# Optimization experiments

Hardware: AMD Instinct MI355X
Metric: run time of the kernel (lower is better)

## Reference

```python
import math
import jax, jax.numpy as jnp
import numpy as np

B, C_IN, H, W = 32, 96, 64, 64
OUT = 128
EXC = int(OUT * 0.8)   # 102 excitatory channels
INH = OUT - EXC        # 26 inhibitory channels
K = 5
PAD = 2                # kernel//2 so all stages keep spatial size


def _sm_kernel(kernel_size=5, sigma_e=1.2, sigma_i=1.4):
    c = kernel_size // 2
    xx, yy = np.meshgrid(np.arange(kernel_size), np.arange(kernel_size), indexing='ij')
    xx = xx.astype(np.float32) - c
    yy = yy.astype(np.float32) - c
    ge = np.exp(-(xx ** 2 + yy ** 2) / (2 * sigma_e ** 2))
    gi = np.exp(-(xx ** 2 + yy ** 2) / (2 * sigma_i ** 2))
    dog = ge / (2 * math.pi * sigma_e ** 2) - gi / (2 * math.pi * sigma_i ** 2)
    dog = dog / dog[c, c]
    return jnp.asarray(dog[None, None], dtype=jnp.float32)  # [1,1,K,K]


def setup_inputs() -> dict:
    key = jax.random.key(0)
    k1, k2, k3, k4 = jax.random.split(key, 4)
    wr = 25.0 / math.sqrt(C_IN * K * K)
    x = jax.random.normal(k1, (B, C_IN, H, W), jnp.float32)
    w_ee = wr * jnp.abs(jax.random.normal(k2, (EXC, C_IN, K, K), jnp.float32))
    w_ei = wr * jnp.abs(jax.random.normal(k3, (INH, EXC, K, K), jnp.float32))
    w_ie = -wr * jnp.abs(jax.random.normal(k4, (EXC, INH, K, K), jnp.float32))
    return {"x": x, "w_ee": w_ee, "w_ei": w_ei, "w_ie": w_ie, "sm_kernel": _sm_kernel()}


def _reflect_pad(x, p):
    if p == 0:
        return x
    return jnp.pad(x, ((0, 0), (0, 0), (p, p), (p, p)), mode='reflect')


def _conv(x, w, pad=0, groups=1):
    return jax.lax.conv_general_dilated(
        x, w, window_strides=(1, 1), padding=[(pad, pad), (pad, pad)],
        dimension_numbers=('NCHW', 'OIHW', 'NCHW'), feature_group_count=groups)


def _forward(x, w_ee, w_ei, w_ie, sm_kernel):
    y_e = _conv(_reflect_pad(x, PAD), w_ee)                 # [B,EXC,H,W], act=Identity
    y_i = jax.nn.relu(_conv(_reflect_pad(y_e, PAD), w_ei))  # [B,INH,H,W]
    y_ie = _conv(_reflect_pad(y_i, PAD), w_ie)              # [B,EXC,H,W]
    y = y_e + y_ie
    # depthwise surround-modulation conv (zero padding, as in F.conv2d)
    w_sm = jnp.tile(sm_kernel, (EXC, 1, 1, 1))              # [EXC,1,K,K]
    y = _conv(y, w_sm, pad=K // 2, groups=EXC)
    return y, y_e, y_i


def reference(x, w_ee, w_ei, w_ie, sm_kernel):
    y, y_e, y_i = _forward(x, w_ee, w_ei, w_ie, sm_kernel)

    # --- hard WTA masks (winner channel per (b,h,w) position) ---
    win_e = jnp.argmax(y_e, axis=1)                                        # [B,H,W]
    mask_e = (jnp.arange(EXC)[None, :, None, None] == win_e[:, None]).astype(y_e.dtype)
    y_wta_e = y_e * mask_e
    win_i = jnp.argmax(jnp.abs(y_i), axis=1)
    mask_i = (jnp.arange(INH)[None, :, None, None] == win_i[:, None]).astype(y_i.dtype)
    y_wta_i = y_i * mask_i

    # --- transpose-conv outer-product trick; with same-size feature maps the
    # conv collapses to a 1x1 full correlation over (b,h,w) -> einsum ---
    yx_ee = jnp.einsum('bchw,behw->ec', x, y_wta_e)[:, :, None, None]      # [EXC,C_IN,1,1]
    yx_ei = jnp.einsum('behw,bihw->ie', y_wta_e, y_wta_i)[:, :, None, None]  # [INH,EXC,1,1]
    yx_ie = jnp.einsum('bihw,behw->ei', y_wta_i, y)[:, :, None, None]      # [EXC,INH,1,1]

    yu_e = jnp.sum(y_wta_e, axis=(0, 2, 3))[:, None, None, None]           # [EXC,1,1,1]
    yu_i = jnp.sum(jnp.abs(y_wta_i), axis=(0, 2, 3))[:, None, None, None]  # [INH,1,1,1]

    upd_ee = yx_ee - yu_e * w_ee   # broadcasts to [EXC,C_IN,K,K]
    upd_ei = yx_ei - yu_i * w_ei
    upd_ie = yx_ie - yu_e * w_ie
    upd_ee = upd_ee / (jnp.abs(upd_ee).max() + 1e-8)
    upd_ei = upd_ei / (jnp.abs(upd_ei).max() + 1e-8)
    upd_ie = upd_ie / (jnp.abs(upd_ie).max() + 1e-8)

    return (y, upd_ee, upd_ei, upd_ie)
```

## Files before the change

### kernel.cpp

```cpp
#include <hip/hip_runtime.h>

#define B_    32
#define CIN_  96
#define EXC_  102
#define INH_  26
#define HH    64
#define WW    64
#define HW_   4096
#define NPOS  (B_*HW_)

typedef short bf8 __attribute__((ext_vector_type(8)));
typedef float f32x4 __attribute__((ext_vector_type(4)));

__device__ __forceinline__ int refl(int i) {
    if (i < 0) i = -i;
    if (i > 63) i = 126 - i;
    return i;
}

__device__ __forceinline__ short f2bf(float f) {
    unsigned u = __float_as_uint(f);
    return (short)((u + 0x7fffu + ((u >> 16) & 1u)) >> 16);
}

template<int C, int CPAD>
__global__ __launch_bounds__(256) void pack_nhwc(
    const float* __restrict__ src, short* __restrict__ dst)
{
    const int b = blockIdx.z;
    const int pos = blockIdx.x*64 + (threadIdx.x & 63);
    const int cg0 = threadIdx.x >> 6;
    for (int cg = cg0; cg < CPAD/8; cg += 4) {
        bf8 v;
#pragma unroll
        for (int j = 0; j < 8; ++j) {
            int c = cg*8 + j;
            float f = (c < C) ? src[((size_t)b*C + c)*HW_ + pos] : 0.f;
            v[j] = f2bf(f);
        }
        *(bf8*)(&dst[((size_t)b*HW_ + pos)*CPAD + cg*8]) = v;
    }
}

template<int N, int C, int NPAD, int CPAD>
__global__ void pack_w(const float* __restrict__ src, short* __restrict__ dst)
{
    int idx = blockIdx.x*256 + threadIdx.x;
    if (idx >= 25*NPAD*CPAD) return;
    int tap = idx / (NPAD*CPAD);
    int rem = idx - tap*NPAD*CPAD;
    int n = rem / CPAD, c = rem - n*CPAD;
    float f = (n < N && c < C) ? src[((size_t)n*C + c)*25 + tap] : 0.f;
    dst[idx] = f2bf(f);
}

template<int CPAD, int NPAD, int NT, int COUT, int NCHUNK, bool RELU, bool ADDIN>
__global__ __launch_bounds__(256, 2) void conv_mfma(
    const short* __restrict__ src, const short* __restrict__ wgt,
    const float* __restrict__ addin, float* __restrict__ out)
{
    __shared__ __align__(16) short sA[400*40];
    const int t  = threadIdx.x;
    const int bx = blockIdx.x;
    const int b  = blockIdx.z;
    const int h0 = (bx >> 2) * 16;
    const int w0 = (bx &  3) * 16;
    const int lane = t & 63;
    const int wv = t >> 6;
    const int nh = lane & 15;
    const int q  = lane >> 4;

    int goff[7], loff[7];
#pragma unroll
    for (int s = 0; s < 7; ++s) {
        int i = t + 256*s;
        if (i < 1600) {
            int rec = i >> 2, seg = i & 3;
            int lh = rec / 20, lw = rec - lh*20;
            int gh = refl(h0 - 2 + lh), gw = refl(w0 - 2 + lw);
            goff[s] = (b*HW_ + gh*WW + gw) * CPAD + seg*8;
            loff[s] = rec*40 + seg*8;
        } else { goff[s] = 0; loff[s] = -1; }
    }

    f32x4 acc[4][NT];
#pragma unroll
    for (int mt = 0; mt < 4; ++mt)
#pragma unroll
        for (int nt = 0; nt < NT; ++nt) {
            f32x4 z = {0.f, 0.f, 0.f, 0.f};
            acc[mt][nt] = z;
        }

    int abase[4];
#pragma unroll
    for (int mt = 0; mt < 4; ++mt)
        abase[mt] = ((wv*4 + mt)*20 + nh)*40 + q*8;

    for (int ck = 0; ck < NCHUNK; ++ck) {
        const int c0 = ck*32;
        __syncthreads();
#pragma unroll
        for (int s = 0; s < 7; ++s)
            if (loff[s] >= 0)
                *(bf8*)(&sA[loff[s]]) = *(const bf8*)(&src[goff[s] + c0]);
        __syncthreads();
        const short* wch = wgt + c0 + nh*CPAD + q*8;
        for (int dh = 0; dh < 5; ++dh) {
#pragma unroll
            for (int dw = 0; dw < 5; ++dw) {
                const int tap = dh*5 + dw;
                bf8 bfr[NT];
#pragma unroll
                for (int nt = 0; nt < NT; ++nt)
                    bfr[nt] = *(const bf8*)(&wch[(size_t)(tap*NPAD + nt*16)*CPAD]);
                bf8 afr[4];
#pragma unroll
                for (int mt = 0; mt < 4; ++mt)
                    afr[mt] = *(const bf8*)(&sA[abase[mt] + (dh*20 + dw)*40]);
#pragma unroll
                for (int mt = 0; mt < 4; ++mt)
#pragma unroll
                    for (int nt = 0; nt < NT; ++nt)
                        acc[mt][nt] = __builtin_amdgcn_mfma_f32_16x16x32_bf16(
                            afr[mt], bfr[nt], acc[mt][nt], 0, 0, 0);
            }
        }
    }

#pragma unroll
    for (int mt = 0; mt < 4; ++mt) {
        const int rowi = h0 + wv*4 + mt;
#pragma unroll
        for (int nt = 0; nt < NT; ++nt) {
            const int chn = nt*16 + nh;
            if (chn < COUT) {
                size_t obase = ((size_t)(b*COUT + chn))*HW_ + rowi*WW + w0 + q*4;
#pragma unroll
                for (int r = 0; r < 4; ++r) {
                    float v = acc[mt][nt][r];
                    if (RELU) v = fmaxf(v, 0.f);
                    if (ADDIN) v += addin[obase + r];
                    out[obase + r] = v;
                }
            }
        }
    }
}

__global__ __launch_bounds__(256) void smconv_v2(
    const float* __restrict__ in, const float* __restrict__ sm,
    float* __restrict__ out)
{
    __shared__ __align__(16) float sx[36*36];
    const int tid = threadIdx.x;
    const int tile = blockIdx.x;
    const int e = blockIdx.y;
    const int b = blockIdx.z;
    const int h0 = (tile >> 1) * 32, w0 = (tile & 1) * 32;
    const int r  = tid >> 3;
    const int cg = (tid & 7) * 4;
    const float* inc = in + ((size_t)(b*EXC_ + e))*HW_;
#pragma unroll
    for (int it = 0; it < 6; ++it) {
        int i = tid + it*256;
        if (i < 1296) {
            int lh = i / 36, lw = i - lh*36;
            int gh = h0 - 2 + lh, gw = w0 - 2 + lw;
            float v = 0.f;
            if (gh >= 0 && gh < HH && gw >= 0 && gw < WW) v = inc[gh*WW + gw];
            sx[i] = v;
        }
    }
    __syncthreads();
    float a0 = 0.f, a1 = 0.f, a2 = 0.f, a3 = 0.f;
#pragma unroll
    for (int kh = 0; kh < 5; ++kh) {
        const float4* rowp = (const float4*)(sx + (r + kh)*36 + cg);
        float4 v0 = rowp[0], v1 = rowp[1];
        float xv[8] = {v0.x, v0.y, v0.z, v0.w, v1.x, v1.y, v1.z, v1.w};
#pragma unroll
        for (int kw = 0; kw < 5; ++kw) {
            float wv = sm[kh*5 + kw];
            a0 = fmaf(xv[kw+0], wv, a0);
            a1 = fmaf(xv[kw+1], wv, a1);
            a2 = fmaf(xv[kw+2], wv, a2);
            a3 = fmaf(xv[kw+3], wv, a3);
        }
    }
    size_t oidx = ((size_t)(b*EXC_ + e))*HW_ + (h0 + r)*WW + w0 + cg;
    *(float4*)(out + oidx) = make_float4(a0, a1, a2, a3);
}

__global__ void wta_kernel(const float* __restrict__ in, int* __restrict__ win,
                           float* __restrict__ val, int C, int use_abs)
{
    int p = blockIdx.x*256 + threadIdx.x;
    int b = p >> 12, hw = p & 4095;
    const float* base = in + ((size_t)b*C)*HW_ + hw;
    float bestv = base[0];
    float bestk = use_abs ? fabsf(bestv) : bestv;
    int besti = 0;
    for (int c = 1; c < C; ++c) {
        float v = base[(size_t)c*HW_];
        float key = use_abs ? fabsf(v) : v;
        if (key > bestk) { bestk = key; bestv = v; besti = c; }
    }
    win[p] = besti;
    val[p] = bestv;
}

__global__ __launch_bounds__(256) void scatter_ee_kernel(
    const float* __restrict__ x, const int* __restrict__ win_e,
    const float* __restrict__ val_e, float* __restrict__ yx_ee,
    float* __restrict__ yu_e)
{
    __shared__ float s_yx[EXC_*CIN_];
    __shared__ float s_yu[EXC_];
    for (int i = threadIdx.x; i < EXC_*CIN_; i += 256) s_yx[i] = 0.f;
    if (threadIdx.x < EXC_) s_yu[threadIdx.x] = 0.f;
    __syncthreads();
    int p0 = blockIdx.x * 512;
    for (int it = 0; it < 2; ++it) {
        int p = p0 + it*256 + threadIdx.x;
        int b = p >> 12, hw = p & 4095;
        int wi = win_e[p]; float v = val_e[p];
        atomicAdd(&s_yu[wi], v);
        const float* xb = x + ((size_t)b*CIN_)*HW_ + hw;
        float* row = s_yx + wi*CIN_;
        for (int c = 0; c < CIN_; ++c)
            atomicAdd(&row[c], v * xb[(size_t)c*HW_]);
    }
    __syncthreads();
    for (int i = threadIdx.x; i < EXC_*CIN_; i += 256) atomicAdd(&yx_ee[i], s_yx[i]);
    if (threadIdx.x < EXC_) atomicAdd(&yu_e[threadIdx.x], s_yu[threadIdx.x]);
}

__global__ __launch_bounds__(256) void scatter_ei_kernel(
    const int* __restrict__ win_e, const float* __restrict__ val_e,
    const int* __restrict__ win_i, const float* __restrict__ val_i,
    float* __restrict__ yx_ei, float* __restrict__ yu_i)
{
    __shared__ float s[INH_*EXC_ + INH_];
    for (int i = threadIdx.x; i < INH_*EXC_ + INH_; i += 256) s[i] = 0.f;
    __syncthreads();
    int p0 = blockIdx.x * 1024;
    for (int it = 0; it < 4; ++it) {
        int p = p0 + it*256 + threadIdx.x;
        int we = win_e[p]; float ve = val_e[p];
        int wi = win_i[p]; float vi = val_i[p];
        atomicAdd(&s[wi*EXC_ + we], ve*vi);
        atomicAdd(&s[INH_*EXC_ + wi], fabsf(vi));
    }
    __syncthreads();
    for (int i = threadIdx.x; i < INH_*EXC_ + INH_; i += 256) {
        float v = s[i];
        if (v != 0.f) {
            if (i < INH_*EXC_) atomicAdd(&yx_ei[i], v);
            else               atomicAdd(&yu_i[i - INH_*EXC_], v);
        }
    }
}

__global__ __launch_bounds__(256) void scatter_ie_kernel(
    const float* __restrict__ y, const int* __restrict__ win_i,
    const float* __restrict__ val_i, float* __restrict__ yx_ie)
{
    __shared__ float s[EXC_*INH_];
    for (int i = threadIdx.x; i < EXC_*INH_; i += 256) s[i] = 0.f;
    __syncthreads();
    int p0 = blockIdx.x * 512;
    for (int it = 0; it < 2; ++it) {
        int p = p0 + it*256 + threadIdx.x;
        int b = p >> 12, hw = p & 4095;
        int wi = win_i[p]; float v = val_i[p];
        if (v != 0.f) {
            const float* yb = y + ((size_t)b*EXC_)*HW_ + hw;
            for (int e = 0; e < EXC_; ++e)
                atomicAdd(&s[e*INH_ + wi], v * yb[(size_t)e*HW_]);
        }
    }
    __syncthreads();
    for (int i = threadIdx.x; i < EXC_*INH_; i += 256) atomicAdd(&yx_ie[i], s[i]);
}

__global__ void upd_absmax_kernel(const float* __restrict__ yx,
    const float* __restrict__ yu, const float* __restrict__ w,
    int E, int C, unsigned int* __restrict__ amax)
{
    __shared__ unsigned int sm_;
    if (threadIdx.x == 0) sm_ = 0u;
    __syncthreads();
    int n = E*C*25;
    float m = 0.f;
    for (int idx = blockIdx.x*256 + threadIdx.x; idx < n; idx += gridDim.x*256) {
        int ec = idx / 25;
        int e = ec / C;
        float v = yx[ec] - yu[e]*w[idx];
        m = fmaxf(m, fabsf(v));
    }
    atomicMax(&sm_, __float_as_uint(m));
    __syncthreads();
    if (threadIdx.x == 0) atomicMax(amax, sm_);
}

__global__ void upd_write_kernel(const float* __restrict__ yx,
    const float* __restrict__ yu, const float* __restrict__ w,
    int E, int C, const unsigned int* __restrict__ amax,
    float* __restrict__ out)
{
    int n = E*C*25;
    int idx = blockIdx.x*256 + threadIdx.x;
    if (idx >= n) return;
    int ec = idx / 25;
    int e = ec / C;
    float v = yx[ec] - yu[e]*w[idx];
    float mx = __uint_as_float(*amax);
    out[idx] = v / (mx + 1e-8f);
}

extern "C" void kernel_launch(void* const* d_in, const int* in_sizes, int n_in,
                              void* d_out, int out_size, void* d_ws, size_t ws_size,
                              hipStream_t stream)
{
    const float* x    = (const float*)d_in[0];
    const float* w_ee = (const float*)d_in[1];
    const float* w_ei = (const float*)d_in[2];
    const float* w_ie = (const float*)d_in[3];
    const float* smk  = (const float*)d_in[4];
    float* out = (float*)d_out;

    float* y_e = (float*)d_ws;
    float* y_i = y_e + (size_t)B_*EXC_*HW_;
    short* R   = (short*)(y_i + (size_t)B_*INH_*HW_);
    short* wee = R + (size_t)16777216;
    short* wei = wee + 268800;
    short* wie = wei + 102400;
    int*   win_e = (int*)(wie + 89600);
    float* val_e = (float*)(win_e + NPOS);
    int*   win_i = (int*)(val_e + NPOS);
    float* val_i = (float*)(win_i + NPOS);
    float* yx_ee = val_i + NPOS;
    float* yx_ei = yx_ee + EXC_*CIN_;
    float* yx_ie = yx_ei + INH_*EXC_;
    float* yu_e  = yx_ie + EXC_*INH_;
    float* yu_i  = yu_e + EXC_;
    unsigned int* amax = (unsigned int*)(yu_i + INH_);

    hipMemsetAsync(yx_ee, 0,
        (size_t)(EXC_*CIN_ + INH_*EXC_ + EXC_*INH_ + EXC_ + INH_ + 3)*sizeof(float),
        stream);

    pack_w<EXC_, CIN_, 112, 96><<<(25*112*96 + 255)/256, 256, 0, stream>>>(w_ee, wee);
    pack_w<INH_, EXC_, 32, 128><<<(25*32*128 + 255)/256, 256, 0, stream>>>(w_ei, wei);
    pack_w<EXC_, INH_, 112, 32><<<(25*112*32 + 255)/256, 256, 0, stream>>>(w_ie, wie);
    pack_nhwc<CIN_, 96><<<dim3(64, 1, B_), 256, 0, stream>>>(x, R);

    conv_mfma<96, 112, 7, EXC_, 3, false, false>
        <<<dim3(16, 1, B_), 256, 0, stream>>>(R, wee, nullptr, y_e);
    wta_kernel<<<NPOS/256, 256, 0, stream>>>(y_e, win_e, val_e, EXC_, 0);

    pack_nhwc<EXC_, 128><<<dim3(64, 1, B_), 256, 0, stream>>>(y_e, R);
    conv_mfma<128, 32, 2, INH_, 4, true, false>
        <<<dim3(16, 1, B_), 256, 0, stream>>>(R, wei, nullptr, y_i);
    wta_kernel<<<NPOS/256, 256, 0, stream>>>(y_i, win_i, val_i, INH_, 1);

    pack_nhwc<INH_, 32><<<dim3(64, 1, B_), 256, 0, stream>>>(y_i, R);
    conv_mfma<32, 112, 7, EXC_, 1, false, true>
        <<<dim3(16, 1, B_), 256, 0, stream>>>(R, wie, y_e, y_e);

    smconv_v2<<<dim3(4, EXC_, B_), 256, 0, stream>>>(y_e, smk, out);

    scatter_ee_kernel<<<256, 256, 0, stream>>>(x, win_e, val_e, yx_ee, yu_e);
    scatter_ei_kernel<<<128, 256, 0, stream>>>(win_e, val_e, win_i, val_i, yx_ei, yu_i);
    scatter_ie_kernel<<<256, 256, 0, stream>>>(out, win_i, val_i, yx_ie);

    upd_absmax_kernel<<<240, 256, 0, stream>>>(yx_ee, yu_e, w_ee, EXC_, CIN_, amax+0);
    upd_absmax_kernel<<<240, 256, 0, stream>>>(yx_ei, yu_i, w_ei, INH_, EXC_, amax+1);
    upd_absmax_kernel<<<240, 256, 0, stream>>>(yx_ie, yu_e, w_ie, EXC_, INH_, amax+2);

    float* out_ee = out + (size_t)B_*EXC_*HW_;
    float* out_ei = out_ee + EXC_*CIN_*25;
    float* out_ie = out_ei + INH_*EXC_*25;
    upd_write_kernel<<<(EXC_*CIN_*25+255)/256, 256, 0, stream>>>(yx_ee, yu_e, w_ee, EXC_, CIN_, amax+0, out_ee);
    upd_write_kernel<<<(INH_*EXC_*25+255)/256, 256, 0, stream>>>(yx_ei, yu_i, w_ei, INH_, EXC_, amax+1, out_ei);
    upd_write_kernel<<<(EXC_*INH_*25+255)/256, 256, 0, stream>>>(yx_ie, yu_e, w_ie, EXC_, INH_, amax+2, out_ie);
}
```

Measured before the change: 593.0 us.

## Fuse bf16 NHWC repack into conv epilogues and split output channels across blocks

Each conv now writes a bf16 NHWC copy of its output directly from the epilogue, which removes the separate pack_nhwc passes for y_e and y_i. Output channels are padded to 128 and split across two blocks in grid.y (NT 7→4), and the launch bound asks for 4 blocks per SM to raise occupancy. The bf16 stores are scattered 2-byte writes with channel stride, which may be poorly coalesced. The A-tile load and im2col work are now repeated for each channel half.

```diff
diff --git a/kernel.cpp b/kernel.cpp
--- a/kernel.cpp
+++ b/kernel.cpp
@@ -54,14 +54,17 @@
     dst[idx] = f2bf(f);
 }
 
-template<int CPAD, int NPAD, int NT, int COUT, int NCHUNK, bool RELU, bool ADDIN>
-__global__ __launch_bounds__(256, 2) void conv_mfma(
+template<int CPAD, int NSTRIDE, int NT, int COUT, int NCHUNK,
+         bool RELU, bool ADDIN, bool BF16OUT, int BFCPAD>
+__global__ __launch_bounds__(256, 4) void conv_mfma(
     const short* __restrict__ src, const short* __restrict__ wgt,
-    const float* __restrict__ addin, float* __restrict__ out)
+    const float* __restrict__ addin, float* __restrict__ out,
+    short* __restrict__ bfout)
 {
     __shared__ __align__(16) short sA[400*40];
     const int t  = threadIdx.x;
     const int bx = blockIdx.x;
+    const int nbase = blockIdx.y * NT * 16;
     const int b  = blockIdx.z;
     const int h0 = (bx >> 2) * 16;
     const int w0 = (bx &  3) * 16;
@@ -105,7 +108,7 @@
             if (loff[s] >= 0)
                 *(bf8*)(&sA[loff[s]]) = *(const bf8*)(&src[goff[s] + c0]);
         __syncthreads();
-        const short* wch = wgt + c0 + nh*CPAD + q*8;
+        const short* wch = wgt + c0 + (nbase + nh)*CPAD + q*8;
         for (int dh = 0; dh < 5; ++dh) {
 #pragma unroll
             for (int dw = 0; dw < 5; ++dw) {
@@ -113,7 +116,7 @@
                 bf8 bfr[NT];
 #pragma unroll
                 for (int nt = 0; nt < NT; ++nt)
-                    bfr[nt] = *(const bf8*)(&wch[(size_t)(tap*NPAD + nt*16)*CPAD]);
+                    bfr[nt] = *(const bf8*)(&wch[(size_t)(tap*NSTRIDE + nt*16)*CPAD]);
                 bf8 afr[4];
 #pragma unroll
                 for (int mt = 0; mt < 4; ++mt)
@@ -133,16 +136,20 @@
         const int rowi = h0 + wv*4 + mt;
 #pragma unroll
         for (int nt = 0; nt < NT; ++nt) {
-            const int chn = nt*16 + nh;
-            if (chn < COUT) {
-                size_t obase = ((size_t)(b*COUT + chn))*HW_ + rowi*WW + w0 + q*4;
-#pragma unroll
-                for (int r = 0; r < 4; ++r) {
-                    float v = acc[mt][nt][r];
-                    if (RELU) v = fmaxf(v, 0.f);
-                    if (ADDIN) v += addin[obase + r];
-                    out[obase + r] = v;
+            const int chn = nbase + nt*16 + nh;
+            const int pbase = rowi*WW + w0 + q*4;
+#pragma unroll
+            for (int r = 0; r < 4; ++r) {
+                float v = acc[mt][nt][r];
+                if (RELU) v = fmaxf(v, 0.f);
+                if (chn < COUT) {
+                    size_t oidx = ((size_t)(b*COUT + chn))*HW_ + pbase + r;
+                    float vo = v;
+                    if (ADDIN) vo += addin[oidx];
+                    out[oidx] = vo;
                 }
+                if (BF16OUT)
+                    bfout[((size_t)b*HW_ + pbase + r)*BFCPAD + chn] = f2bf(v);
             }
         }
     }
@@ -330,13 +337,17 @@
     const float* smk  = (const float*)d_in[4];
     float* out = (float*)d_out;
 
-    float* y_e = (float*)d_ws;
-    float* y_i = y_e + (size_t)B_*EXC_*HW_;
-    short* R   = (short*)(y_i + (size_t)B_*INH_*HW_);
-    short* wee = R + (size_t)16777216;
-    short* wei = wee + 268800;
-    short* wie = wei + 102400;
-    int*   win_e = (int*)(wie + 89600);
+    float* y_e  = (float*)d_ws;
+    short* yebf = (short*)(y_e + (size_t)B_*EXC_*HW_);
+    float* xreg = (float*)(yebf + (size_t)16777216);
+    short* xbf  = (short*)xreg;
+    float* y_i  = xreg;
+    short* yibf = (short*)(xreg + (size_t)B_*INH_*HW_);
+    short* wee  = (short*)(xreg + (size_t)12582912/2*2/2 + 6291456);
+    wee = (short*)(xreg + 6291456);
+    short* wei = wee + 25*128*96;
+    short* wie = wei + 25*32*128;
+    int*   win_e = (int*)(wie + 25*128*32);
     float* val_e = (float*)(win_e + NPOS);
     int*   win_i = (int*)(val_e + NPOS);
     float* val_i = (float*)(win_i + NPOS);
@@ -351,23 +362,21 @@
         (size_t)(EXC_*CIN_ + INH_*EXC_ + EXC_*INH_ + EXC_ + INH_ + 3)*sizeof(float),
         stream);
 
-    pack_w<EXC_, CIN_, 112, 96><<<(25*112*96 + 255)/256, 256, 0, stream>>>(w_ee, wee);
+    pack_w<EXC_, CIN_, 128, 96><<<(25*128*96 + 255)/256, 256, 0, stream>>>(w_ee, wee);
     pack_w<INH_, EXC_, 32, 128><<<(25*32*128 + 255)/256, 256, 0, stream>>>(w_ei, wei);
-    pack_w<EXC_, INH_, 112, 32><<<(25*112*32 + 255)/256, 256, 0, stream>>>(w_ie, wie);
-    pack_nhwc<CIN_, 96><<<dim3(64, 1, B_), 256, 0, stream>>>(x, R);
-
-    conv_mfma<96, 112, 7, EXC_, 3, false, false>
-        <<<dim3(16, 1, B_), 256, 0, stream>>>(R, wee, nullptr, y_e);
+    pack_w<EXC_, INH_, 128, 32><<<(25*128*32 + 255)/256, 256, 0, stream>>>(w_ie, wie);
+    pack_nhwc<CIN_, 96><<<dim3(64, 1, B_), 256, 0, stream>>>(x, xbf);
+
+    conv_mfma<96, 128, 4, EXC_, 3, false, false, true, 128>
+        <<<dim3(16, 2, B_), 256, 0, stream>>>(xbf, wee, nullptr, y_e, yebf);
     wta_kernel<<<NPOS/256, 256, 0, stream>>>(y_e, win_e, val_e, EXC_, 0);
 
-    pack_nhwc<EXC_, 128><<<dim3(64, 1, B_), 256, 0, stream>>>(y_e, R);
-    conv_mfma<128, 32, 2, INH_, 4, true, false>
-        <<<dim3(16, 1, B_), 256, 0, stream>>>(R, wei, nullptr, y_i);
+    conv_mfma<128, 32, 2, INH_, 4, true, false, true, 32>
+        <<<dim3(16, 1, B_), 256, 0, stream>>>(yebf, wei, nullptr, y_i, yibf);
     wta_kernel<<<NPOS/256, 256, 0, stream>>>(y_i, win_i, val_i, INH_, 1);
 
-    pack_nhwc<INH_, 32><<<dim3(64, 1, B_), 256, 0, stream>>>(y_i, R);
-    conv_mfma<32, 112, 7, EXC_, 1, false, true>
-        <<<dim3(16, 1, B_), 256, 0, stream>>>(R, wie, y_e, y_e);
+    conv_mfma<32, 128, 4, EXC_, 1, false, true, false, 1>
+        <<<dim3(16, 2, B_), 256, 0, stream>>>(yibf, wie, y_e, y_e, nullptr);
 
     smconv_v2<<<dim3(4, EXC_, B_), 256, 0, stream>>>(y_e, smk, out);
 
```

Result: slower. 618.4 us (+4.3%).
